# Performance work log

Measured on AMD Instinct MI355X. Metric: run time of the kernel, lower is better.

Reference implementation:

```python
import jax, jax.numpy as jnp
import numpy as np

B, T, DM = 1, 8192, 1024
DS, DC, EXP = 16, 4, 2
DI = DM * EXP  # 2048


def setup_inputs() -> dict:
    key = jax.random.key(0)
    ks = jax.random.split(key, 6)
    sc = lambda k, shape, s: jax.random.normal(k, shape, jnp.float32) * s
    return {
        "x": jax.random.normal(ks[0], (B, T, DM), jnp.float32),
        "W_in": sc(ks[1], (DM, 2 * DI), 0.02),        # stored [in, out]
        "conv_w": sc(ks[2], (DI, 1, DC), 0.2),        # depthwise conv weight (OIH)
        "conv_b": jnp.zeros((DI,), jnp.float32),
        "W_x": sc(ks[3], (DI, 2 * DS + 1), 0.02),     # stored [in, out]
        "A_log": jnp.log(jnp.arange(1, DS + 1, dtype=jnp.float32)),
        "D": jnp.ones((DI,), jnp.float32),
        "W_out": sc(ks[4], (DI, DM), 0.02),           # stored [in, out]
    }


def reference(x, W_in, conv_w, conv_b, W_x, A_log, D, W_out):
    Bq, Tq, _ = x.shape
    # input projection and gate split
    xz = x @ W_in                              # [B,T,2*DI]
    xc, z = jnp.split(xz, 2, axis=-1)          # each [B,T,DI]
    # causal depthwise conv1d (pad left DC-1 == torch pad both + truncate [:T])
    xcT = jnp.transpose(xc, (0, 2, 1))         # [B,DI,T]
    conv = jax.lax.conv_general_dilated(
        xcT, conv_w, window_strides=(1,), padding=[(DC - 1, 0)],
        feature_group_count=DI)
    conv = conv + conv_b[None, :, None]
    xs = jax.nn.silu(jnp.transpose(conv, (0, 2, 1)))   # [B,T,DI]
    # selective SSM parameters (single shared delta per timestep)
    x_dbl = xs @ W_x                           # [B,T,2N+1]
    delta = jax.nn.softplus(x_dbl[..., :1])    # [B,T,1]
    Bp = x_dbl[..., 1:1 + DS]                  # [B,T,N]
    Cp = x_dbl[..., 1 + DS:]                   # [B,T,N]
    A = -jnp.exp(A_log)                        # [N]
    A_bar = jnp.exp(delta * A)                 # [B,T,N]
    B_bar = delta * Bp                         # [B,T,N]

    def step(h, inp):
        a_t, b_t, x_t, c_t = inp               # [B,N],[B,N],[B,DI],[B,N]
        h = a_t[:, None, :] * h + b_t[:, None, :] * x_t[:, :, None]  # [B,DI,N]
        y_t = jnp.einsum('bdn,bn->bd', h, c_t)
        return h, y_t

    h0 = jnp.zeros((Bq, DI, DS), xs.dtype)
    seq = (jnp.swapaxes(A_bar, 0, 1), jnp.swapaxes(B_bar, 0, 1),
           jnp.swapaxes(xs, 0, 1), jnp.swapaxes(Cp, 0, 1))
    _, ys = jax.lax.scan(step, h0, seq)        # ys: [T,B,DI]
    y = jnp.swapaxes(ys, 0, 1) + D * xs        # [B,T,DI]
    y = y * jax.nn.silu(z)
    return y @ W_out                           # [B,T,DM]
```

## Files before the change

kernel.cpp:

```cpp
#include <hip/hip_runtime.h>
#include <hip/hip_bf16.h>

#define T_SEQ 8192
#define DMODEL 1024
#define DINNER 2048
#define NSTATE 16
#define NCH 128
#define CL 64

typedef __attribute__((ext_vector_type(8))) short bf16x8;
typedef __attribute__((ext_vector_type(4))) float f32x4;

__device__ __forceinline__ float bf2f(ushort u) {
  union { unsigned u; float f; } c; c.u = ((unsigned)u) << 16; return c.f;
}
__device__ __forceinline__ ushort f2bf(float f) {
  union { float f; unsigned u; } c; c.f = f;
  unsigned r = c.u + 0x7FFFu + ((c.u >> 16) & 1u);
  return (ushort)(r >> 16);
}

#define GLD16(dst, src) __builtin_amdgcn_global_load_lds( \
    (const __attribute__((address_space(1))) void*)(src), \
    (__attribute__((address_space(3))) void*)(dst), 16, 0, 0)

template<int N> __device__ __forceinline__ void waitcnt_vm() {
  asm volatile("s_waitcnt vmcnt(%0)" :: "i"(N) : "memory");
}
#define LGKM0() do { asm volatile("s_waitcnt lgkmcnt(0)" ::: "memory"); \
                     __builtin_amdgcn_sched_barrier(0); } while (0)
#define BAR() do { __builtin_amdgcn_s_barrier(); \
                   __builtin_amdgcn_sched_barrier(0); } while (0)

__global__ __launch_bounds__(256) void prep_all(const float* __restrict__ x,
                                                const float* __restrict__ W_in,
                                                const float* __restrict__ W_out,
                                                const float* __restrict__ Wx,
                                                ushort* __restrict__ xbf,
                                                ushort* __restrict__ winT,
                                                ushort* __restrict__ woutT,
                                                ushort* __restrict__ wxT) {
  __shared__ float tile[32][33];
  int b = blockIdx.x, tid = threadIdx.x;
  if (b < 8192) {
    int i = b * 256 + tid;
    float4 v = ((const float4*)x)[i];
    ushort4 o;
    o.x = f2bf(v.x); o.y = f2bf(v.y); o.z = f2bf(v.z); o.w = f2bf(v.w);
    ((ushort4*)xbf)[i] = o;
    return;
  }
  b -= 8192;
  const float* in; ushort* out; int R, C, bx, by;
  if (b < 4096)      { in = W_in;  out = winT;  R = 1024; C = 4096; bx = b & 127; by = b >> 7; }
  else if (b < 6144) { b -= 4096; in = W_out; out = woutT; R = 2048; C = 1024; bx = b & 31; by = b >> 5; }
  else {
    int idx = (b - 6144) * 256 + tid;
    int j = idx >> 11, k = idx & 2047;
    wxT[idx] = (j < 33) ? f2bf(Wx[k * 33 + j]) : (ushort)0;
    return;
  }
  int xx = tid & 31, yy = tid >> 5;
  bx *= 32; by *= 32;
#pragma unroll
  for (int j = 0; j < 32; j += 8)
    tile[yy + j][xx] = in[(size_t)(by + yy + j) * C + bx + xx];
  __syncthreads();
#pragma unroll
  for (int j = 0; j < 32; j += 8)
    out[(size_t)(bx + yy + j) * R + by + xx] = f2bf(tile[xx][yy + j]);
}

template<int OUTMODE, int MR>
__global__ __launch_bounds__(512, 2)
void gemm8p(const ushort* __restrict__ A, const ushort* __restrict__ B,
            void* __restrict__ out0, void* __restrict__ out1,
            int N, int K, int MX) {
  constexpr int BM = MR * 32;
  constexpr int H = MR / 2;
  constexpr int AHL = BM / 128;
  constexpr int VM = 2 * AHL + 2;
  extern __shared__ __align__(16) char smem[];
  char* const sBr = smem + 2 * BM * 128;

  const int tid = threadIdx.x, lane = tid & 63, wid = tid >> 6;
  const int wm = wid >> 2, wn = wid & 3;
  const int xcd = blockIdx.x & 7, jb = blockIdx.x >> 3;
  const int mtile = xcd * MX + (jb % MX), ntile = jb / MX;
  const int mbase = mtile * BM, nbase = ntile * 256;
  const int NT = K >> 6;

  const int sr = tid >> 3;
  const int scol = ((tid & 7) ^ (sr & 7)) << 3;
  const ushort* pA = A + (size_t)(mbase + sr) * K + scol;
  const ushort* pB = B + (size_t)(nbase + sr) * K + scol;

  auto stgA = [&](int buf, int h, int tt) {
#pragma unroll
    for (int r = 0; r < AHL; ++r)
      GLD16(smem + buf * (BM * 128) + (h * (BM / 2) + r * 64) * 128 + wid * 1024,
            pA + (size_t)(h * (BM / 2) + r * 64) * K + (size_t)tt * 64);
  };
  auto stgB = [&](int buf, int h, int tt) {
#pragma unroll
    for (int r = 0; r < 2; ++r)
      GLD16(sBr + buf * 32768 + (h * 128 + r * 64) * 128 + wid * 1024,
            pB + (size_t)(h * 128 + r * 64) * K + (size_t)tt * 64);
  };

  const int frow = lane & 15, hh = lane >> 4;
  const int sw[2] = { ((hh) ^ (frow & 7)) << 4, ((4 + hh) ^ (frow & 7)) << 4 };
  const int arow = (wm * (MR * 16) + frow) * 128;
  const int brow = (wn * 64 + frow) * 128;

  f32x4 acc[MR][4];
#pragma unroll
  for (int m = 0; m < MR; ++m)
#pragma unroll
    for (int n = 0; n < 4; ++n) acc[m][n] = (f32x4){0.f, 0.f, 0.f, 0.f};

  stgA(0, 0, 0); stgA(0, 1, 0); stgB(0, 0, 0); stgB(0, 1, 0);
  if (NT > 1) { stgA(1, 0, 1); stgA(1, 1, 1); stgB(1, 0, 1); }
  waitcnt_vm<VM>();
  BAR();

  for (int t = 0; t < NT; ++t) {
    const int b = t & 1;
    const char* bA = smem + b * (BM * 128);
    const char* bB = sBr + b * 32768;
    bf16x8 alo[H][2], ahi[H][2], b01[2][2], b23[2][2];

#pragma unroll
    for (int m = 0; m < H; ++m)
#pragma unroll
      for (int kk = 0; kk < 2; ++kk)
        alo[m][kk] = *(const bf16x8*)(bA + arow + m * 2048 + sw[kk]);
#pragma unroll
    for (int n = 0; n < 2; ++n)
#pragma unroll
      for (int kk = 0; kk < 2; ++kk)
        b01[n][kk] = *(const bf16x8*)(bB + brow + n * 2048 + sw[kk]);
    if (t + 1 < NT) stgB((t + 1) & 1, 1, t + 1);
    BAR(); LGKM0();
    __builtin_amdgcn_s_setprio(1);
#pragma unroll
    for (int m = 0; m < H; ++m)
#pragma unroll
      for (int n = 0; n < 2; ++n)
#pragma unroll
        for (int kk = 0; kk < 2; ++kk)
          acc[m][n] = __builtin_amdgcn_mfma_f32_16x16x32_bf16(alo[m][kk], b01[n][kk], acc[m][n], 0, 0, 0);
    __builtin_amdgcn_s_setprio(0);
    BAR();

#pragma unroll
    for (int m = 0; m < H; ++m)
#pragma unroll
      for (int kk = 0; kk < 2; ++kk)
        ahi[m][kk] = *(const bf16x8*)(bA + arow + (H + m) * 2048 + sw[kk]);
    BAR(); LGKM0();
    __builtin_amdgcn_s_setprio(1);
#pragma unroll
    for (int m = 0; m < H; ++m)
#pragma unroll
      for (int n = 0; n < 2; ++n)
#pragma unroll
        for (int kk = 0; kk < 2; ++kk)
          acc[H + m][n] = __builtin_amdgcn_mfma_f32_16x16x32_bf16(ahi[m][kk], b01[n][kk], acc[H + m][n], 0, 0, 0);
    __builtin_amdgcn_s_setprio(0);
    BAR();

#pragma unroll
    for (int n = 0; n < 2; ++n)
#pragma unroll
      for (int kk = 0; kk < 2; ++kk)
        b23[n][kk] = *(const bf16x8*)(bB + brow + (2 + n) * 2048 + sw[kk]);
    if (t + 2 < NT) stgA(b, 0, t + 2);
    BAR(); LGKM0();
    __builtin_amdgcn_s_setprio(1);
#pragma unroll
    for (int m = 0; m < H; ++m)
#pragma unroll
      for (int n = 0; n < 2; ++n)
#pragma unroll
        for (int kk = 0; kk < 2; ++kk)
          acc[H + m][2 + n] = __builtin_amdgcn_mfma_f32_16x16x32_bf16(ahi[m][kk], b23[n][kk], acc[H + m][2 + n], 0, 0, 0);
    __builtin_amdgcn_s_setprio(0);
    BAR();

    if (t + 2 < NT) { stgA(b, 1, t + 2); stgB(b, 0, t + 2); }
    __builtin_amdgcn_s_setprio(1);
#pragma unroll
    for (int m = 0; m < H; ++m)
#pragma unroll
      for (int n = 0; n < 2; ++n)
#pragma unroll
        for (int kk = 0; kk < 2; ++kk)
          acc[m][2 + n] = __builtin_amdgcn_mfma_f32_16x16x32_bf16(alo[m][kk], b23[n][kk], acc[m][2 + n], 0, 0, 0);
    __builtin_amdgcn_s_setprio(0);
    if (t + 2 < NT) waitcnt_vm<VM>(); else waitcnt_vm<0>();
    BAR();
  }

  const int crow0 = mbase + wm * (MR * 16) + (lane >> 4) * 4;
  const int ccol0 = wn * 64 + (lane & 15);
  if (OUTMODE == 0) {
    float* po = (float*)out0;
#pragma unroll
    for (int m = 0; m < MR; ++m)
#pragma unroll
      for (int n = 0; n < 4; ++n)
#pragma unroll
        for (int j = 0; j < 4; ++j)
          po[(size_t)(crow0 + m * 16 + j) * N + nbase + ccol0 + n * 16] = acc[m][n][j];
  } else {
    ushort* dst = (nbase < 2048) ? (ushort*)out0 : (ushort*)out1;
    const int cbase = (nbase & 2047) + ccol0;
#pragma unroll
    for (int m = 0; m < MR; ++m)
#pragma unroll
      for (int n = 0; n < 4; ++n)
#pragma unroll
        for (int j = 0; j < 4; ++j)
          dst[(size_t)(crow0 + m * 16 + j) * 2048 + cbase + n * 16] = f2bf(acc[m][n][j]);
  }
}

__global__ __launch_bounds__(256) void gemm_thin(const ushort* __restrict__ A,
                                                 const ushort* __restrict__ Bw,
                                                 float* __restrict__ part) {
  __shared__ __align__(16) ushort sA[128 * 64];
  __shared__ __align__(16) ushort sB[48 * 64];
  const int tid = threadIdx.x, lane = tid & 63, wid = tid >> 6;
  const int mbase = blockIdx.x * 128;
  const int kbase = blockIdx.y * 512;
  const int frow = lane & 15, fke = (lane >> 4) * 8;

  f32x4 acc[2][3];
#pragma unroll
  for (int m = 0; m < 2; ++m)
#pragma unroll
    for (int n = 0; n < 3; ++n) acc[m][n] = (f32x4){0.f, 0.f, 0.f, 0.f};

  for (int k0 = 0; k0 < 512; k0 += 64) {
#pragma unroll
    for (int j = 0; j < 4; ++j) {
      int o = tid * 16 + j * 4096;
      int row = o >> 7, ke = ((o >> 4) & 7) * 8;
      GLD16((char*)sA + wid * 1024 + j * 4096,
            A + (size_t)(mbase + row) * DINNER + kbase + k0 + ke);
    }
    for (int i = tid; i < 384; i += 256) {
      int brow = i >> 3, kc = (i & 7) * 8;
      *(bf16x8*)&sB[brow * 64 + kc] = *(const bf16x8*)(Bw + (size_t)brow * DINNER + kbase + k0 + kc);
    }
    __syncthreads();
    bf16x8 af[2][2], bf_[3][2];
#pragma unroll
    for (int m = 0; m < 2; ++m)
#pragma unroll
      for (int ks = 0; ks < 2; ++ks)
        af[m][ks] = *(const bf16x8*)&sA[(wid * 32 + m * 16 + frow) * 64 + ks * 32 + fke];
#pragma unroll
    for (int n = 0; n < 3; ++n)
#pragma unroll
      for (int ks = 0; ks < 2; ++ks)
        bf_[n][ks] = *(const bf16x8*)&sB[(n * 16 + frow) * 64 + ks * 32 + fke];
#pragma unroll
    for (int m = 0; m < 2; ++m)
#pragma unroll
      for (int n = 0; n < 3; ++n)
#pragma unroll
        for (int ks = 0; ks < 2; ++ks)
          acc[m][n] = __builtin_amdgcn_mfma_f32_16x16x32_bf16(af[m][ks], bf_[n][ks], acc[m][n], 0, 0, 0);
    __syncthreads();
  }
  float* po = part + (size_t)blockIdx.y * (T_SEQ * 48);
#pragma unroll
  for (int m = 0; m < 2; ++m)
#pragma unroll
    for (int n = 0; n < 3; ++n)
#pragma unroll
      for (int j = 0; j < 4; ++j) {
        int rr = mbase + wid * 32 + m * 16 + (lane >> 4) * 4 + j;
        int cc = n * 16 + (lane & 15);
        po[(size_t)rr * 48 + cc] = acc[m][n][j];
      }
}

__global__ __launch_bounds__(256) void conv_silu(const ushort* __restrict__ xc,
                                                 const float* __restrict__ cw,
                                                 const float* __restrict__ cb,
                                                 ushort* __restrict__ xs) {
  int idx = blockIdx.x * 256 + threadIdx.x;
  int t = idx >> 11, d = idx & 2047;
  float4 w = *(const float4*)(cw + d * 4);
  float a = cb[d];
  const float wk[4] = {w.x, w.y, w.z, w.w};
#pragma unroll
  for (int k = 0; k < 4; ++k) {
    int tt = t - 3 + k;
    if (tt >= 0) a += bf2f(xc[(size_t)tt * 2048 + d]) * wk[k];
  }
  float s = a / (1.f + expf(-a));
  xs[idx] = f2bf(s);
}

__global__ __launch_bounds__(256) void precompute_k(const float* __restrict__ part,
                                                    const float* __restrict__ A_log,
                                                    float* __restrict__ abar,
                                                    float* __restrict__ bbar,
                                                    float* __restrict__ cc,
                                                    float* __restrict__ P) {
  __shared__ float ld[256 * 33];
  const int t0 = blockIdx.x * 256, tid = threadIdx.x;
  for (int i = tid; i < 256 * 33; i += 256) {
    int r = i / 33, col = i - r * 33;
    size_t off = (size_t)(t0 + r) * 48 + col;
    ld[i] = part[off] + part[(size_t)T_SEQ * 48 + off] +
            part[2 * (size_t)T_SEQ * 48 + off] + part[3 * (size_t)T_SEQ * 48 + off];
  }
  __syncthreads();
  const float* r = &ld[tid * 33];
  float v = r[0];
  float delta = (v > 20.f) ? v : log1pf(expf(v));
  int t = t0 + tid;
#pragma unroll
  for (int n = 0; n < NSTATE; ++n) {
    float A = -expf(A_log[n]);
    abar[t * 16 + n] = expf(delta * A);
    bbar[t * 16 + n] = delta * r[1 + n];
    cc[t * 16 + n]   = r[17 + n];
  }
  float s = delta;
#pragma unroll
  for (int off = 32; off > 0; off >>= 1) s += __shfl_down(s, off);
  s = __shfl(s, 0);
  int lane = tid & 63, c = blockIdx.x * 4 + (tid >> 6);
  if (lane < 16) P[c * 16 + lane] = expf(-expf(A_log[lane]) * s);
}

__global__ __launch_bounds__(256) void scan1(const ushort* __restrict__ xs,
                                             const float* __restrict__ abar,
                                             const float* __restrict__ bbar,
                                             ushort* __restrict__ hend) {
  int c = blockIdx.x;
  int d = blockIdx.y * 256 + threadIdx.x;
  __shared__ float s_ab[CL * 16], s_bb[CL * 16];
  for (int e = threadIdx.x; e < CL * 16; e += 256) {
    s_ab[e] = abar[(size_t)c * CL * 16 + e];
    s_bb[e] = bbar[(size_t)c * CL * 16 + e];
  }
  __syncthreads();
  float h[16];
#pragma unroll
  for (int n = 0; n < 16; ++n) h[n] = 0.f;
  int tbase = c * CL;
  for (int i = 0; i < CL; ++i) {
    float x = bf2f(xs[(size_t)(tbase + i) * DINNER + d]);
#pragma unroll
    for (int n = 0; n < 16; ++n) h[n] = s_ab[i * 16 + n] * h[n] + s_bb[i * 16 + n] * x;
  }
  ushort* o = hend + ((size_t)c * DINNER + d) * 16;
  bf16x8 o0, o1;
#pragma unroll
  for (int q = 0; q < 8; ++q) { o0[q] = (short)f2bf(h[q]); o1[q] = (short)f2bf(h[8 + q]); }
  *(bf16x8*)o = o0;
  *(bf16x8*)(o + 8) = o1;
}

__global__ __launch_bounds__(128) void scan2(const ushort* __restrict__ hend,
                                             const float* __restrict__ P,
                                             ushort* __restrict__ hin) {
  int idx = blockIdx.x * 128 + threadIdx.x;
  int n = idx & 15;
  float h = 0.f;
  for (int g = 0; g < 16; ++g) {
    float e[8], p[8];
#pragma unroll
    for (int j = 0; j < 8; ++j) {
      e[j] = bf2f(hend[(size_t)(g * 8 + j) * 32768 + idx]);
      p[j] = P[(g * 8 + j) * 16 + n];
    }
#pragma unroll
    for (int j = 0; j < 8; ++j) {
      hin[(size_t)(g * 8 + j) * 32768 + idx] = f2bf(h);
      h = p[j] * h + e[j];
    }
  }
}

__global__ __launch_bounds__(256) void scan3(const ushort* __restrict__ xs,
                                             const ushort* __restrict__ zb,
                                             const float* __restrict__ abar,
                                             const float* __restrict__ bbar,
                                             const float* __restrict__ cc,
                                             const ushort* __restrict__ hin,
                                             const float* __restrict__ Dv,
                                             ushort* __restrict__ y) {
  int c = blockIdx.x;
  int d = blockIdx.y * 256 + threadIdx.x;
  __shared__ float s_ab[CL * 16], s_bb[CL * 16], s_cc[CL * 16];
  for (int e = threadIdx.x; e < CL * 16; e += 256) {
    s_ab[e] = abar[(size_t)c * CL * 16 + e];
    s_bb[e] = bbar[(size_t)c * CL * 16 + e];
    s_cc[e] = cc[(size_t)c * CL * 16 + e];
  }
  __syncthreads();
  float h[16];
  const ushort* hi = hin + ((size_t)c * DINNER + d) * 16;
  bf16x8 h0 = *(const bf16x8*)hi, h1 = *(const bf16x8*)(hi + 8);
#pragma unroll
  for (int q = 0; q < 8; ++q) { h[q] = bf2f((ushort)h0[q]); h[8 + q] = bf2f((ushort)h1[q]); }
  float Dd = Dv[d];
  int tbase = c * CL;
  for (int i = 0; i < CL; ++i) {
    size_t t = tbase + i;
    float x = bf2f(xs[t * DINNER + d]);
    float ys = 0.f;
#pragma unroll
    for (int n = 0; n < 16; ++n) {
      h[n] = s_ab[i * 16 + n] * h[n] + s_bb[i * 16 + n] * x;
      ys += s_cc[i * 16 + n] * h[n];
    }
    float z = bf2f(zb[t * 2048 + d]);
    float yv = (ys + Dd * x) * (z / (1.f + expf(-z)));
    y[t * DINNER + d] = f2bf(yv);
  }
}

extern "C" void kernel_launch(void* const* d_in, const int* in_sizes, int n_in,
                              void* d_out, int out_size, void* d_ws, size_t ws_size,
                              hipStream_t stream) {
  const float* x      = (const float*)d_in[0];
  const float* W_in   = (const float*)d_in[1];
  const float* conv_w = (const float*)d_in[2];
  const float* conv_b = (const float*)d_in[3];
  const float* W_x    = (const float*)d_in[4];
  const float* A_log  = (const float*)d_in[5];
  const float* Dv     = (const float*)d_in[6];
  const float* W_out  = (const float*)d_in[7];
  float* out = (float*)d_out;

  char* w = (char*)d_ws;
  auto alloc = [&](size_t bytes) { char* p = w; w += (bytes + 255) & ~(size_t)255; return p; };

  ushort* xbf   = (ushort*)alloc((size_t)T_SEQ * DMODEL * 2);
  ushort* winT  = (ushort*)alloc((size_t)4096 * 1024 * 2);
  ushort* woutT = (ushort*)alloc((size_t)1024 * 2048 * 2);
  ushort* wxT   = (ushort*)alloc((size_t)48 * 2048 * 2);
  ushort* xc    = (ushort*)alloc((size_t)T_SEQ * DINNER * 2);
  ushort* zb    = (ushort*)alloc((size_t)T_SEQ * DINNER * 2);
  ushort* xs    = (ushort*)alloc((size_t)T_SEQ * DINNER * 2);
  float*  parts = (float*) alloc((size_t)4 * T_SEQ * 48 * 4);
  float*  abar  = (float*) alloc((size_t)T_SEQ * 16 * 4);
  float*  bbar  = (float*) alloc((size_t)T_SEQ * 16 * 4);
  float*  ccb   = (float*) alloc((size_t)T_SEQ * 16 * 4);
  float*  P     = (float*) alloc((size_t)NCH * 16 * 4);
  ushort* hend  = (ushort*)alloc((size_t)NCH * DINNER * 16 * 2);
  ushort* hin   = (ushort*)alloc((size_t)NCH * DINNER * 16 * 2);
  ushort* ybf   = (ushort*)alloc((size_t)T_SEQ * DINNER * 2);

  auto kg1 = gemm8p<1, 8>;
  auto kg3 = gemm8p<0, 4>;
  hipFuncSetAttribute(reinterpret_cast<const void*>(kg1),
                      hipFuncAttributeMaxDynamicSharedMemorySize, 131072);
  hipFuncSetAttribute(reinterpret_cast<const void*>(kg3),
                      hipFuncAttributeMaxDynamicSharedMemorySize, 98304);

  prep_all<<<dim3(14720), 256, 0, stream>>>(x, W_in, W_out, W_x, xbf, winT, woutT, wxT);

  kg1<<<dim3(512), 512, 131072, stream>>>(xbf, winT, xc, zb, 4096, 1024, 4);

  conv_silu<<<(T_SEQ * DINNER) / 256, 256, 0, stream>>>(xc, conv_w, conv_b, xs);

  gemm_thin<<<dim3(T_SEQ / 128, 4), 256, 0, stream>>>(xs, wxT, parts);

  precompute_k<<<32, 256, 0, stream>>>(parts, A_log, abar, bbar, ccb, P);

  scan1<<<dim3(NCH, DINNER / 256), 256, 0, stream>>>(xs, abar, bbar, hend);
  scan2<<<256, 128, 0, stream>>>(hend, P, hin);
  scan3<<<dim3(NCH, DINNER / 256), 256, 0, stream>>>(xs, zb, abar, bbar, ccb, hin, Dv, ybf);

  kg3<<<dim3(256), 512, 98304, stream>>>(ybf, woutT, out, nullptr, 1024, 2048, 8);
}
```

Baseline: 285.2 us.

## Restructure GEMM main loop into K-split phases with reordered A/B prefetch

The 8-wave GEMM inner loop is reorganized so each iteration walks the 64-wide K tile in two halves, loading A fragments for the low and high row halves and all four B fragments per half, instead of splitting by N columns. The A half-rows each wave owns are remapped to sit in separate BM/2 halves of shared memory, and the global-to-LDS prefetch schedule changes so the next A high half is issued early and B is fetched with the A low half two tiles ahead, with new wait counts. The aim is to cut fragment register pressure and balance memory issue against MFMA phases. The risk is the subtler wait-count bookkeeping and a changed output row mapping.

```diff
diff --git a/kernel.cpp b/kernel.cpp
--- a/kernel.cpp
+++ b/kernel.cpp
@@ -79,7 +79,7 @@
   constexpr int BM = MR * 32;
   constexpr int H = MR / 2;
   constexpr int AHL = BM / 128;
-  constexpr int VM = 2 * AHL + 2;
+  constexpr int VMs = 2 * AHL + 4;
   extern __shared__ __align__(16) char smem[];
   char* const sBr = smem + 2 * BM * 128;
 
@@ -110,7 +110,8 @@
 
   const int frow = lane & 15, hh = lane >> 4;
   const int sw[2] = { ((hh) ^ (frow & 7)) << 4, ((4 + hh) ^ (frow & 7)) << 4 };
-  const int arow = (wm * (MR * 16) + frow) * 128;
+  const int arow_lo = (wm * (H * 16) + frow) * 128;
+  const int arow_hi = ((BM / 2) + wm * (H * 16) + frow) * 128;
   const int brow = (wn * 64 + frow) * 128;
 
   f32x4 acc[MR][4];
@@ -120,109 +121,100 @@
     for (int n = 0; n < 4; ++n) acc[m][n] = (f32x4){0.f, 0.f, 0.f, 0.f};
 
   stgA(0, 0, 0); stgA(0, 1, 0); stgB(0, 0, 0); stgB(0, 1, 0);
-  if (NT > 1) { stgA(1, 0, 1); stgA(1, 1, 1); stgB(1, 0, 1); }
-  waitcnt_vm<VM>();
+  if (NT > 1) { stgA(1, 0, 1); stgB(1, 0, 1); stgB(1, 1, 1); }
+  waitcnt_vm<AHL + 4>();
   BAR();
 
   for (int t = 0; t < NT; ++t) {
     const int b = t & 1;
     const char* bA = smem + b * (BM * 128);
     const char* bB = sBr + b * 32768;
-    bf16x8 alo[H][2], ahi[H][2], b01[2][2], b23[2][2];
-
-#pragma unroll
-    for (int m = 0; m < H; ++m)
-#pragma unroll
-      for (int kk = 0; kk < 2; ++kk)
-        alo[m][kk] = *(const bf16x8*)(bA + arow + m * 2048 + sw[kk]);
-#pragma unroll
-    for (int n = 0; n < 2; ++n)
-#pragma unroll
-      for (int kk = 0; kk < 2; ++kk)
-        b01[n][kk] = *(const bf16x8*)(bB + brow + n * 2048 + sw[kk]);
-    if (t + 1 < NT) stgB((t + 1) & 1, 1, t + 1);
+    bf16x8 af[H], bf[4];
+
+#pragma unroll
+    for (int m = 0; m < H; ++m) af[m] = *(const bf16x8*)(bA + arow_lo + m * 2048 + sw[0]);
+#pragma unroll
+    for (int n = 0; n < 4; ++n) bf[n] = *(const bf16x8*)(bB + brow + n * 2048 + sw[0]);
+    if (t + 1 < NT) stgA(b ^ 1, 1, t + 1);
     BAR(); LGKM0();
     __builtin_amdgcn_s_setprio(1);
 #pragma unroll
     for (int m = 0; m < H; ++m)
 #pragma unroll
-      for (int n = 0; n < 2; ++n)
-#pragma unroll
-        for (int kk = 0; kk < 2; ++kk)
-          acc[m][n] = __builtin_amdgcn_mfma_f32_16x16x32_bf16(alo[m][kk], b01[n][kk], acc[m][n], 0, 0, 0);
+      for (int n = 0; n < 4; ++n)
+        acc[m][n] = __builtin_amdgcn_mfma_f32_16x16x32_bf16(af[m], bf[n], acc[m][n], 0, 0, 0);
+    __builtin_amdgcn_s_setprio(0);
+    if (t + 1 < NT) waitcnt_vm<VMs>(); else waitcnt_vm<0>();
+    BAR();
+
+#pragma unroll
+    for (int m = 0; m < H; ++m) af[m] = *(const bf16x8*)(bA + arow_hi + m * 2048 + sw[0]);
+    BAR(); LGKM0();
+    __builtin_amdgcn_s_setprio(1);
+#pragma unroll
+    for (int m = 0; m < H; ++m)
+#pragma unroll
+      for (int n = 0; n < 4; ++n)
+        acc[H + m][n] = __builtin_amdgcn_mfma_f32_16x16x32_bf16(af[m], bf[n], acc[H + m][n], 0, 0, 0);
     __builtin_amdgcn_s_setprio(0);
     BAR();
 
 #pragma unroll
-    for (int m = 0; m < H; ++m)
-#pragma unroll
-      for (int kk = 0; kk < 2; ++kk)
-        ahi[m][kk] = *(const bf16x8*)(bA + arow + (H + m) * 2048 + sw[kk]);
+    for (int m = 0; m < H; ++m) af[m] = *(const bf16x8*)(bA + arow_lo + m * 2048 + sw[1]);
+#pragma unroll
+    for (int n = 0; n < 4; ++n) bf[n] = *(const bf16x8*)(bB + brow + n * 2048 + sw[1]);
     BAR(); LGKM0();
     __builtin_amdgcn_s_setprio(1);
 #pragma unroll
     for (int m = 0; m < H; ++m)
 #pragma unroll
-      for (int n = 0; n < 2; ++n)
-#pragma unroll
-        for (int kk = 0; kk < 2; ++kk)
-          acc[H + m][n] = __builtin_amdgcn_mfma_f32_16x16x32_bf16(ahi[m][kk], b01[n][kk], acc[H + m][n], 0, 0, 0);
+      for (int n = 0; n < 4; ++n)
+        acc[m][n] = __builtin_amdgcn_mfma_f32_16x16x32_bf16(af[m], bf[n], acc[m][n], 0, 0, 0);
     __builtin_amdgcn_s_setprio(0);
     BAR();
 
 #pragma unroll
-    for (int n = 0; n < 2; ++n)
-#pragma unroll
-      for (int kk = 0; kk < 2; ++kk)
-        b23[n][kk] = *(const bf16x8*)(bB + brow + (2 + n) * 2048 + sw[kk]);
-    if (t + 2 < NT) stgA(b, 0, t + 2);
+    for (int m = 0; m < H; ++m) af[m] = *(const bf16x8*)(bA + arow_hi + m * 2048 + sw[1]);
+    if (t + 2 < NT) { stgA(b, 0, t + 2); stgB(b, 0, t + 2); stgB(b, 1, t + 2); }
     BAR(); LGKM0();
     __builtin_amdgcn_s_setprio(1);
 #pragma unroll
     for (int m = 0; m < H; ++m)
 #pragma unroll
-      for (int n = 0; n < 2; ++n)
-#pragma unroll
-        for (int kk = 0; kk < 2; ++kk)
-          acc[H + m][2 + n] = __builtin_amdgcn_mfma_f32_16x16x32_bf16(ahi[m][kk], b23[n][kk], acc[H + m][2 + n], 0, 0, 0);
+      for (int n = 0; n < 4; ++n)
+        acc[H + m][n] = __builtin_amdgcn_mfma_f32_16x16x32_bf16(af[m], bf[n], acc[H + m][n], 0, 0, 0);
     __builtin_amdgcn_s_setprio(0);
+    if (t + 2 < NT)      waitcnt_vm<VMs>();
+    else if (t + 1 < NT) waitcnt_vm<AHL>();
     BAR();
-
-    if (t + 2 < NT) { stgA(b, 1, t + 2); stgB(b, 0, t + 2); }
-    __builtin_amdgcn_s_setprio(1);
-#pragma unroll
-    for (int m = 0; m < H; ++m)
-#pragma unroll
-      for (int n = 0; n < 2; ++n)
-#pragma unroll
-        for (int kk = 0; kk < 2; ++kk)
-          acc[m][2 + n] = __builtin_amdgcn_mfma_f32_16x16x32_bf16(alo[m][kk], b23[n][kk], acc[m][2 + n], 0, 0, 0);
-    __builtin_amdgcn_s_setprio(0);
-    if (t + 2 < NT) waitcnt_vm<VM>(); else waitcnt_vm<0>();
-    BAR();
-  }
-
-  const int crow0 = mbase + wm * (MR * 16) + (lane >> 4) * 4;
-  const int ccol0 = wn * 64 + (lane & 15);
+  }
+
+  const int rbase0 = mbase + wm * (H * 16) + (lane >> 4) * 4;
+  const int rbase1 = mbase + BM / 2 + wm * (H * 16) + (lane >> 4) * 4;
+  const int ccol0 = nbase + wn * 64 + (lane & 15);
   if (OUTMODE == 0) {
     float* po = (float*)out0;
 #pragma unroll
-    for (int m = 0; m < MR; ++m)
+    for (int m = 0; m < MR; ++m) {
+      int r0 = (m < H) ? (rbase0 + m * 16) : (rbase1 + (m - H) * 16);
 #pragma unroll
       for (int n = 0; n < 4; ++n)
 #pragma unroll
         for (int j = 0; j < 4; ++j)
-          po[(size_t)(crow0 + m * 16 + j) * N + nbase + ccol0 + n * 16] = acc[m][n][j];
+          po[(size_t)(r0 + j) * N + ccol0 - nbase + nbase + n * 16] = acc[m][n][j];
+    }
   } else {
     ushort* dst = (nbase < 2048) ? (ushort*)out0 : (ushort*)out1;
-    const int cbase = (nbase & 2047) + ccol0;
-#pragma unroll
-    for (int m = 0; m < MR; ++m)
+    const int cbase = ((nbase & 2047) + wn * 64 + (lane & 15));
+#pragma unroll
+    for (int m = 0; m < MR; ++m) {
+      int r0 = (m < H) ? (rbase0 + m * 16) : (rbase1 + (m - H) * 16);
 #pragma unroll
       for (int n = 0; n < 4; ++n)
 #pragma unroll
         for (int j = 0; j < 4; ++j)
-          dst[(size_t)(crow0 + m * 16 + j) * 2048 + cbase + n * 16] = f2bf(acc[m][n][j]);
+          dst[(size_t)(r0 + j) * 2048 + cbase + n * 16] = f2bf(acc[m][n][j]);
+    }
   }
 }
 
```

New measurement: 298.0 us. 4.5% more time.

## Split-K the output projection GEMM with larger tiles and a reduction pass

Applied to the files above, without the earlier changes.

The final projection GEMM now uses a 256-row tile variant (MR=8) and splits K=2048 into two halves across blockIdx.y. Each half writes fp32 partials into the reused xc buffer, and a new reduce2 kernel sums them into the output. The aim is to keep the larger, more reuse-efficient tiles while still launching enough blocks to fill the GPU. The cost is an extra kernel launch plus roughly 64MB of partial-result traffic written and read back.

```diff
diff --git a/kernel.cpp b/kernel.cpp
--- a/kernel.cpp
+++ b/kernel.cpp
@@ -75,7 +75,7 @@
 __global__ __launch_bounds__(512, 2)
 void gemm8p(const ushort* __restrict__ A, const ushort* __restrict__ B,
             void* __restrict__ out0, void* __restrict__ out1,
-            int N, int K, int MX) {
+            int N, int K, int LDK, int MX, size_t poff) {
   constexpr int BM = MR * 32;
   constexpr int H = MR / 2;
   constexpr int AHL = BM / 128;
@@ -89,23 +89,26 @@
   const int mtile = xcd * MX + (jb % MX), ntile = jb / MX;
   const int mbase = mtile * BM, nbase = ntile * 256;
   const int NT = K >> 6;
+  const int ks = blockIdx.y;
+  A += (size_t)ks * K;
+  B += (size_t)ks * K;
 
   const int sr = tid >> 3;
   const int scol = ((tid & 7) ^ (sr & 7)) << 3;
-  const ushort* pA = A + (size_t)(mbase + sr) * K + scol;
-  const ushort* pB = B + (size_t)(nbase + sr) * K + scol;
+  const ushort* pA = A + (size_t)(mbase + sr) * LDK + scol;
+  const ushort* pB = B + (size_t)(nbase + sr) * LDK + scol;
 
   auto stgA = [&](int buf, int h, int tt) {
 #pragma unroll
     for (int r = 0; r < AHL; ++r)
       GLD16(smem + buf * (BM * 128) + (h * (BM / 2) + r * 64) * 128 + wid * 1024,
-            pA + (size_t)(h * (BM / 2) + r * 64) * K + (size_t)tt * 64);
+            pA + (size_t)(h * (BM / 2) + r * 64) * LDK + (size_t)tt * 64);
   };
   auto stgB = [&](int buf, int h, int tt) {
 #pragma unroll
     for (int r = 0; r < 2; ++r)
       GLD16(sBr + buf * 32768 + (h * 128 + r * 64) * 128 + wid * 1024,
-            pB + (size_t)(h * 128 + r * 64) * K + (size_t)tt * 64);
+            pB + (size_t)(h * 128 + r * 64) * LDK + (size_t)tt * 64);
   };
 
   const int frow = lane & 15, hh = lane >> 4;
@@ -205,7 +208,7 @@
   const int crow0 = mbase + wm * (MR * 16) + (lane >> 4) * 4;
   const int ccol0 = wn * 64 + (lane & 15);
   if (OUTMODE == 0) {
-    float* po = (float*)out0;
+    float* po = (float*)out0 + (size_t)ks * poff;
 #pragma unroll
     for (int m = 0; m < MR; ++m)
 #pragma unroll
@@ -224,6 +227,17 @@
         for (int j = 0; j < 4; ++j)
           dst[(size_t)(crow0 + m * 16 + j) * 2048 + cbase + n * 16] = f2bf(acc[m][n][j]);
   }
+}
+
+__global__ __launch_bounds__(256) void reduce2(const float* __restrict__ p,
+                                               float* __restrict__ o) {
+  int i = blockIdx.x * 256 + threadIdx.x;
+  float4 a = ((const float4*)p)[i];
+  float4 b = ((const float4*)p)[i + 2097152];
+  o[4 * (size_t)i + 0] = a.x + b.x;
+  o[4 * (size_t)i + 1] = a.y + b.y;
+  o[4 * (size_t)i + 2] = a.z + b.z;
+  o[4 * (size_t)i + 3] = a.w + b.w;
 }
 
 __global__ __launch_bounds__(256) void gemm_thin(const ushort* __restrict__ A,
@@ -461,16 +475,18 @@
   ushort* hin   = (ushort*)alloc((size_t)NCH * DINNER * 16 * 2);
   ushort* ybf   = (ushort*)alloc((size_t)T_SEQ * DINNER * 2);
 
+  float* parts3 = (float*)xc;
+
   auto kg1 = gemm8p<1, 8>;
-  auto kg3 = gemm8p<0, 4>;
+  auto kg3 = gemm8p<0, 8>;
   hipFuncSetAttribute(reinterpret_cast<const void*>(kg1),
                       hipFuncAttributeMaxDynamicSharedMemorySize, 131072);
   hipFuncSetAttribute(reinterpret_cast<const void*>(kg3),
-                      hipFuncAttributeMaxDynamicSharedMemorySize, 98304);
+                      hipFuncAttributeMaxDynamicSharedMemorySize, 131072);
 
   prep_all<<<dim3(14720), 256, 0, stream>>>(x, W_in, W_out, W_x, xbf, winT, woutT, wxT);
 
-  kg1<<<dim3(512), 512, 131072, stream>>>(xbf, winT, xc, zb, 4096, 1024, 4);
+  kg1<<<dim3(512, 1), 512, 131072, stream>>>(xbf, winT, xc, zb, 4096, 1024, 1024, 4, 0);
 
   conv_silu<<<(T_SEQ * DINNER) / 256, 256, 0, stream>>>(xc, conv_w, conv_b, xs);
 
@@ -482,5 +498,8 @@
   scan2<<<256, 128, 0, stream>>>(hend, P, hin);
   scan3<<<dim3(NCH, DINNER / 256), 256, 0, stream>>>(xs, zb, abar, bbar, ccb, hin, Dv, ybf);
 
-  kg3<<<dim3(256), 512, 98304, stream>>>(ybf, woutT, out, nullptr, 1024, 2048, 8);
-}
+  kg3<<<dim3(128, 2), 512, 131072, stream>>>(ybf, woutT, parts3, nullptr,
+                                             1024, 1024, 2048, 4, (size_t)T_SEQ * 1024);
+
+  reduce2<<<(T_SEQ * 1024 / 4) / 256, 256, 0, stream>>>(parts3, out);
+}
```

New measurement: 301.9 us. 1.06x slower.
